# Kernel tuning notes

Measured on AMD Instinct MI355X. Metric: run time of the kernel, lower is better.

Reference implementation:

```python
import jax, jax.numpy as jnp
import numpy as np

N_NODES = 100000
N_EDGES = 1600000
IN_DIM = 256
OUT_DIM = 128


def setup_inputs() -> dict:
    key = jax.random.key(0)
    k1, k2, k3, k4, k5 = jax.random.split(key, 5)
    inputs = jax.random.normal(k1, (N_NODES, IN_DIM), dtype=jnp.float32)
    # xavier_uniform with relu gain, as in the torch init
    gain = float(np.sqrt(2.0))
    limit = gain * float(np.sqrt(6.0 / (IN_DIM + OUT_DIM)))
    W = jax.random.uniform(k2, (IN_DIM, OUT_DIM), dtype=jnp.float32,
                           minval=-limit, maxval=limit)
    edge_src = jax.random.randint(k3, (N_EDGES,), 0, N_NODES, dtype=jnp.int32)
    edge_dst = jax.random.randint(k4, (N_EDGES,), 0, N_NODES, dtype=jnp.int32)
    edge_val = jax.random.uniform(k5, (N_EDGES,), dtype=jnp.float32)
    return {"inputs": inputs, "W": W, "edge_src": edge_src,
            "edge_dst": edge_dst, "edge_val": edge_val}


def reference(inputs, W, edge_src, edge_dst, edge_val):
    # x = inputs @ W  (dense GEMM)
    h = inputs @ W                                  # [N, OUT_DIM]
    # adj @ h  as SpMM over COO edges: out[d] += val * h[s]
    msg = edge_val[:, None] * h[edge_src]           # [E, OUT_DIM]
    agg = jax.ops.segment_sum(msg, edge_dst, num_segments=N_NODES)
    # act = ReLU, fused with SpMM output
    return jax.nn.relu(agg)
```

## Files before the change

### kernel.cpp

```cpp
#include <hip/hip_runtime.h>
#include <hip/hip_bf16.h>

#define N_NODES 100000
#define N_EDGES 1600000
#define IN_DIM  256
#define OUT_DIM 128

#define GEMM_ROWS   64
#define GEMM_BLOCKS ((N_NODES + GEMM_ROWS - 1) / GEMM_ROWS)

#define NBUCK   196
#define BSHIFT  9
#define BCAP    10240
#define BSTRIDE 16
#define EPB     2048
#define BIN_BLOCKS ((N_EDGES + EPB - 1) / EPB)

typedef __attribute__((ext_vector_type(8))) short bf16x8;
typedef __attribute__((ext_vector_type(4))) float f32x4;

__device__ __forceinline__ ushort f2bf(float f) {
    union { float f; unsigned u; } v; v.f = f;
    unsigned r = v.u + 0x7FFF + ((v.u >> 16) & 1);
    return (ushort)(r >> 16);
}
__device__ __forceinline__ float bflo(unsigned u) {
    union { unsigned u; float f; } v; v.u = u << 16; return v.f;
}
__device__ __forceinline__ float bfhi(unsigned u) {
    union { unsigned u; float f; } v; v.u = u & 0xFFFF0000u; return v.f;
}

__global__ __launch_bounds__(256) void pack_w(const float* __restrict__ W,
                                              ushort* __restrict__ Wp) {
    const int t = blockIdx.x * 256 + threadIdx.x;
    if (t >= 4096) return;
    const int kk = t >> 9, n = (t >> 6) & 7, l = t & 63;
    const int kbase = kk * 32 + (l >> 4) * 8;
    const int col   = n * 16 + (l & 15);
    ushort* o = Wp + (size_t)t * 8;
#pragma unroll
    for (int j = 0; j < 8; ++j)
        o[j] = f2bf(W[(size_t)(kbase + j) * OUT_DIM + col]);
}

__global__ __launch_bounds__(256) void gemm_coarse(const float* __restrict__ X,
                                                   const bf16x8* __restrict__ Bp,
                                                   ushort* __restrict__ H,
                                                   const int* __restrict__ esrc,
                                                   const int* __restrict__ edst,
                                                   const float* __restrict__ eval,
                                                   int* __restrict__ bcur,
                                                   int2* __restrict__ binned) {
    __shared__ ushort xt[GEMM_ROWS * IN_DIM];

    if (blockIdx.x >= GEMM_BLOCKS) {
        int*   cnt   = (int*)xt;
        int*   lbase = (int*)xt + 256;
        int*   sbase = (int*)xt + 512;
        int*   cur   = (int*)xt + 768;
        int2*  lrec  = (int2*)((char*)xt + 4096);
        unsigned char* lbid = (unsigned char*)xt + 20480;

        const int blk = blockIdx.x - GEMM_BLOCKS;
        const int cb  = blk * EPB;
        const int lim = (N_EDGES - cb < EPB) ? (N_EDGES - cb) : EPB;
        const int tid = threadIdx.x;
        const int lane = tid & 63, wv = tid >> 6;

        if (tid < NBUCK) cnt[tid] = 0;
        __syncthreads();
        for (int i = tid; i < lim; i += 256)
            atomicAdd(&cnt[edst[cb + i] >> BSHIFT], 1);
        __syncthreads();

        {
            __shared__ int wsum[4];
            const int v = (tid < NBUCK) ? cnt[tid] : 0;
            int sv = v;
#pragma unroll
            for (int d = 1; d < 64; d <<= 1) {
                const int t = __shfl_up(sv, d, 64);
                if (lane >= d) sv += t;
            }
            if (lane == 63) wsum[wv] = sv;
            __syncthreads();
            int wx = 0;
#pragma unroll
            for (int w = 0; w < 4; ++w) if (w < wv) wx += wsum[w];
            if (tid < NBUCK) {
                const int ex = wx + sv - v;
                lbase[tid] = ex;
                cur[tid]   = ex;
                sbase[tid] = v ? atomicAdd(&bcur[tid * BSTRIDE], v) : 0;
            }
        }
        __syncthreads();

        for (int i = tid; i < lim; i += 256) {
            const int d = edst[cb + i];
            const int b = d >> BSHIFT;
            const int pos = atomicAdd(&cur[b], 1);
            int2 rec;
            rec.x = esrc[cb + i] | ((d & 511) << 20);
            rec.y = __float_as_int(eval[cb + i]);
            lrec[pos] = rec;
            lbid[pos] = (unsigned char)b;
        }
        __syncthreads();

        for (int i = tid; i < lim; i += 256) {
            const int b   = lbid[i];
            const int off = sbase[b] + (i - lbase[b]);
            if (off < BCAP)
                binned[(size_t)b * BCAP + off] = lrec[i];
        }
        return;
    }

    const int row0 = blockIdx.x * GEMM_ROWS;
    const int tid  = threadIdx.x;

    float4 v[16];
#pragma unroll
    for (int it = 0; it < 16; ++it) {
        const int tr = it * 4 + (tid >> 6);
        int grow = row0 + tr; if (grow >= N_NODES) grow = N_NODES - 1;
        v[it] = *reinterpret_cast<const float4*>(X + (size_t)grow * IN_DIM + (tid & 63) * 4);
    }
#pragma unroll
    for (int it = 0; it < 16; ++it) {
        const int tr = it * 4 + (tid >> 6);
        const int tc = (tid & 63) * 4;
        ushort4 b4;
        b4.x = f2bf(v[it].x); b4.y = f2bf(v[it].y);
        b4.z = f2bf(v[it].z); b4.w = f2bf(v[it].w);
        const int byte = (tr * 512 + tc * 2) ^ ((tr & 7) << 4);
        *reinterpret_cast<ushort4*>((char*)xt + byte) = b4;
    }
    __syncthreads();

    const int lane = tid & 63;
    const int wid  = tid >> 6;
    const int wr   = wid >> 1;
    const int wc   = wid & 1;
    const int rlo  = lane & 15;
    const int kseg = lane >> 4;
    const int rl0  = wr * 32 + rlo;
    const int rl1  = rl0 + 16;
    const int rxor = (rlo & 7) << 4;

    f32x4 acc[2][4] = {};

    for (int kk = 0; kk < 8; ++kk) {
        const int cb2 = (kk * 64 + kseg * 16) ^ rxor;
        const bf16x8 A0 = *reinterpret_cast<const bf16x8*>((const char*)xt + rl0 * 512 + cb2);
        const bf16x8 A1 = *reinterpret_cast<const bf16x8*>((const char*)xt + rl1 * 512 + cb2);
        const bf16x8* bbase = Bp + (size_t)(kk * 8 + wc * 4) * 64 + lane;
#pragma unroll
        for (int n = 0; n < 4; ++n) {
            const bf16x8 Bf = bbase[(size_t)n * 64];
            acc[0][n] = __builtin_amdgcn_mfma_f32_16x16x32_bf16(A0, Bf, acc[0][n], 0, 0, 0);
            acc[1][n] = __builtin_amdgcn_mfma_f32_16x16x32_bf16(A1, Bf, acc[1][n], 0, 0, 0);
        }
    }

#pragma unroll
    for (int i = 0; i < 2; ++i) {
#pragma unroll
        for (int r = 0; r < 4; ++r) {
            const int row = row0 + wr * 32 + i * 16 + kseg * 4 + r;
            if (row < N_NODES) {
#pragma unroll
                for (int n = 0; n < 4; ++n)
                    H[(size_t)row * OUT_DIM + (wc * 4 + n) * 16 + rlo] = f2bf(acc[i][n][r]);
            }
        }
    }
}

__global__ __launch_bounds__(256) void scan_buckets(const int* __restrict__ bcur,
                                                    int* __restrict__ gbase) {
    __shared__ int ws[4];
    const int tid = threadIdx.x, lane = tid & 63, wid = tid >> 6;
    const int v = (tid < NBUCK) ? bcur[tid * BSTRIDE] : 0;
    int sv = v;
#pragma unroll
    for (int d = 1; d < 64; d <<= 1) {
        const int t = __shfl_up(sv, d, 64);
        if (lane >= d) sv += t;
    }
    if (lane == 63) ws[wid] = sv;
    __syncthreads();
    int wx = 0;
#pragma unroll
    for (int w = 0; w < 4; ++w) if (w < wid) wx += ws[w];
    if (tid < NBUCK) gbase[tid] = wx + sv - v;
}

__global__ __launch_bounds__(1024) void bin_fine(const int* __restrict__ bcur,
                                                 const int* __restrict__ gbase,
                                                 const int2* __restrict__ binned,
                                                 int* __restrict__ offsets,
                                                 int2* __restrict__ recs) {
    __shared__ int nh[512];
    __shared__ int cur[512];
    __shared__ int ws[4];
    const int b   = blockIdx.x;
    const int tid = threadIdx.x, lane = tid & 63, wid = tid >> 6;
    const int node0 = b << BSHIFT;
    int nn = N_NODES - node0; if (nn > 512) nn = 512;
    int size = bcur[b * BSTRIDE]; if (size > BCAP) size = BCAP;
    const int2* in = binned + (size_t)b * BCAP;
    const int base_out = gbase[b];

    if (tid < 512) nh[tid] = 0;
    __syncthreads();
    for (int k = tid; k < size; k += 1024)
        atomicAdd(&nh[(in[k].x >> 20) & 511], 1);
    __syncthreads();

    int a0 = 0, ts = 0, sv = 0;
    if (tid < 256) {
        a0 = nh[2 * tid];
        const int a1 = nh[2 * tid + 1];
        ts = a0 + a1;
        sv = ts;
#pragma unroll
        for (int d = 1; d < 64; d <<= 1) {
            const int t = __shfl_up(sv, d, 64);
            if (lane >= d) sv += t;
        }
        if (lane == 63) ws[wid] = sv;
    }
    __syncthreads();
    if (tid < 256) {
        int wx = 0;
#pragma unroll
        for (int w = 0; w < 4; ++w) if (w < wid) wx += ws[w];
        const int ex = wx + sv - ts;
        cur[2 * tid]     = base_out + ex;
        cur[2 * tid + 1] = base_out + ex + a0;
        if (2 * tid < nn)     offsets[node0 + 2 * tid]     = base_out + ex;
        if (2 * tid + 1 < nn) offsets[node0 + 2 * tid + 1] = base_out + ex + a0;
    }
    if (b == 0 && tid == 0) offsets[N_NODES] = N_EDGES;
    __syncthreads();

    for (int k = tid; k < size; k += 1024) {
        const int2 r = in[k];
        const int pos = atomicAdd(&cur[(r.x >> 20) & 511], 1);
        int2 o; o.x = r.x & 0xFFFFF; o.y = r.y;
        recs[pos] = o;
    }
}

__global__ __launch_bounds__(256) void spmm_pull(const ushort* __restrict__ H,
                                                 const int* __restrict__ offsets,
                                                 const int2* __restrict__ recs,
                                                 float* __restrict__ out) {
    const int tid   = threadIdx.x;
    const int lane  = tid & 63;
    const int g     = lane >> 4;
    const int c     = lane & 15;
    const int gwave = blockIdx.x * 4 + (tid >> 6);
    const int node  = gwave * 4 + g;
    if (node >= N_NODES) return;

    const int beg = offsets[node];
    const int end = offsets[node + 1];

    float a0 = 0.f, a1 = 0.f, a2 = 0.f, a3 = 0.f;
    float a4 = 0.f, a5 = 0.f, a6 = 0.f, a7 = 0.f;

    int e = beg;
    for (; e + 3 < end; e += 4) {
        const int2 r0 = recs[e + 0];
        const int2 r1 = recs[e + 1];
        const int2 r2 = recs[e + 2];
        const int2 r3 = recs[e + 3];
        const uint4 h0 = *((const uint4*)(H + (size_t)r0.x * OUT_DIM) + c);
        const uint4 h1 = *((const uint4*)(H + (size_t)r1.x * OUT_DIM) + c);
        const uint4 h2 = *((const uint4*)(H + (size_t)r2.x * OUT_DIM) + c);
        const uint4 h3 = *((const uint4*)(H + (size_t)r3.x * OUT_DIM) + c);
        const float v0 = __int_as_float(r0.y), v1 = __int_as_float(r1.y);
        const float v2 = __int_as_float(r2.y), v3 = __int_as_float(r3.y);
        a0 = fmaf(v0, bflo(h0.x), a0);  a1 = fmaf(v0, bfhi(h0.x), a1);
        a2 = fmaf(v0, bflo(h0.y), a2);  a3 = fmaf(v0, bfhi(h0.y), a3);
        a4 = fmaf(v0, bflo(h0.z), a4);  a5 = fmaf(v0, bfhi(h0.z), a5);
        a6 = fmaf(v0, bflo(h0.w), a6);  a7 = fmaf(v0, bfhi(h0.w), a7);
        a0 = fmaf(v1, bflo(h1.x), a0);  a1 = fmaf(v1, bfhi(h1.x), a1);
        a2 = fmaf(v1, bflo(h1.y), a2);  a3 = fmaf(v1, bfhi(h1.y), a3);
        a4 = fmaf(v1, bflo(h1.z), a4);  a5 = fmaf(v1, bfhi(h1.z), a5);
        a6 = fmaf(v1, bflo(h1.w), a6);  a7 = fmaf(v1, bfhi(h1.w), a7);
        a0 = fmaf(v2, bflo(h2.x), a0);  a1 = fmaf(v2, bfhi(h2.x), a1);
        a2 = fmaf(v2, bflo(h2.y), a2);  a3 = fmaf(v2, bfhi(h2.y), a3);
        a4 = fmaf(v2, bflo(h2.z), a4);  a5 = fmaf(v2, bfhi(h2.z), a5);
        a6 = fmaf(v2, bflo(h2.w), a6);  a7 = fmaf(v2, bfhi(h2.w), a7);
        a0 = fmaf(v3, bflo(h3.x), a0);  a1 = fmaf(v3, bfhi(h3.x), a1);
        a2 = fmaf(v3, bflo(h3.y), a2);  a3 = fmaf(v3, bfhi(h3.y), a3);
        a4 = fmaf(v3, bflo(h3.z), a4);  a5 = fmaf(v3, bfhi(h3.z), a5);
        a6 = fmaf(v3, bflo(h3.w), a6);  a7 = fmaf(v3, bfhi(h3.w), a7);
    }
    for (; e < end; ++e) {
        const int2 r0 = recs[e];
        const float v0 = __int_as_float(r0.y);
        const uint4 h0 = *((const uint4*)(H + (size_t)r0.x * OUT_DIM) + c);
        a0 = fmaf(v0, bflo(h0.x), a0);  a1 = fmaf(v0, bfhi(h0.x), a1);
        a2 = fmaf(v0, bflo(h0.y), a2);  a3 = fmaf(v0, bfhi(h0.y), a3);
        a4 = fmaf(v0, bflo(h0.z), a4);  a5 = fmaf(v0, bfhi(h0.z), a5);
        a6 = fmaf(v0, bflo(h0.w), a6);  a7 = fmaf(v0, bfhi(h0.w), a7);
    }

    float* op = out + (size_t)node * OUT_DIM + c * 8;
    float4 o0, o1;
    o0.x = fmaxf(a0, 0.f); o0.y = fmaxf(a1, 0.f);
    o0.z = fmaxf(a2, 0.f); o0.w = fmaxf(a3, 0.f);
    o1.x = fmaxf(a4, 0.f); o1.y = fmaxf(a5, 0.f);
    o1.z = fmaxf(a6, 0.f); o1.w = fmaxf(a7, 0.f);
    *reinterpret_cast<float4*>(op)     = o0;
    *reinterpret_cast<float4*>(op + 4) = o1;
}

extern "C" void kernel_launch(void* const* d_in, const int* in_sizes, int n_in,
                              void* d_out, int out_size, void* d_ws, size_t ws_size,
                              hipStream_t stream) {
    const float* X    = (const float*)d_in[0];
    const float* W    = (const float*)d_in[1];
    const int*   esrc = (const int*)d_in[2];
    const int*   edst = (const int*)d_in[3];
    const float* eval = (const float*)d_in[4];
    float*       out  = (float*)d_out;

    char* ws = (char*)d_ws;
    ushort* Hb     = (ushort*)ws;  ws += (size_t)N_NODES * OUT_DIM * sizeof(ushort);
    ushort* Wp     = (ushort*)ws;  ws += (size_t)4096 * 8 * sizeof(ushort);
    int*    offsets= (int*)ws;     ws += (((size_t)(N_NODES + 1) * 4 + 127) & ~(size_t)127);
    int*    bcur   = (int*)ws;     ws += (size_t)NBUCK * BSTRIDE * 4;
    int*    gbase  = (int*)ws;     ws += ((NBUCK * 4 + 127) & ~127);
    int2*   binned = (int2*)ws;    ws += (size_t)NBUCK * BCAP * sizeof(int2);
    int2*   recs   = (int2*)ws;

    pack_w<<<16, 256, 0, stream>>>(W, Wp);
    hipMemsetAsync(bcur, 0, (size_t)NBUCK * BSTRIDE * 4, stream);
    gemm_coarse<<<GEMM_BLOCKS + BIN_BLOCKS, 256, 0, stream>>>(X, (const bf16x8*)Wp, Hb,
                                                              esrc, edst, eval,
                                                              bcur, binned);

    scan_buckets<<<1, 256, 0, stream>>>(bcur, gbase);
    bin_fine<<<NBUCK, 1024, 0, stream>>>(bcur, gbase, binned, offsets, recs);

    spmm_pull<<<(N_NODES + 15) / 16, 256, 0, stream>>>(Hb, offsets, recs, out);
}
```

Before: 134.4 us.

## Halve GEMM and binning tiles and raise occupancy of the fused kernel

The GEMM tile shrinks from 64 to 32 rows and now uses four waves that each cover 32 output columns, so each block needs less shared memory and fewer registers. Launch bounds now request 8 blocks per SM. The edge-binning blocks process 1024 edges each instead of 2048, with the LDS offsets adjusted to the smaller buffer. The X load loop now streams loads instead of preloading 16 float4s, and row bounds checks are dropped because 32 divides N_NODES exactly. In exchange there are more blocks, more total reads of the packed W, and more binning blocks that each add to the global atomic traffic.

```diff
diff --git a/kernel.cpp b/kernel.cpp
--- a/kernel.cpp
+++ b/kernel.cpp
@@ -6,14 +6,14 @@
 #define IN_DIM  256
 #define OUT_DIM 128
 
-#define GEMM_ROWS   64
-#define GEMM_BLOCKS ((N_NODES + GEMM_ROWS - 1) / GEMM_ROWS)
+#define GEMM_ROWS   32
+#define GEMM_BLOCKS (N_NODES / GEMM_ROWS)
 
 #define NBUCK   196
 #define BSHIFT  9
 #define BCAP    10240
 #define BSTRIDE 16
-#define EPB     2048
+#define EPB     1024
 #define BIN_BLOCKS ((N_EDGES + EPB - 1) / EPB)
 
 typedef __attribute__((ext_vector_type(8))) short bf16x8;
@@ -44,15 +44,15 @@
         o[j] = f2bf(W[(size_t)(kbase + j) * OUT_DIM + col]);
 }
 
-__global__ __launch_bounds__(256) void gemm_coarse(const float* __restrict__ X,
-                                                   const bf16x8* __restrict__ Bp,
-                                                   ushort* __restrict__ H,
-                                                   const int* __restrict__ esrc,
-                                                   const int* __restrict__ edst,
-                                                   const float* __restrict__ eval,
-                                                   int* __restrict__ bcur,
-                                                   int2* __restrict__ binned) {
-    __shared__ ushort xt[GEMM_ROWS * IN_DIM];
+__global__ __launch_bounds__(256, 8) void gemm_coarse(const float* __restrict__ X,
+                                                      const bf16x8* __restrict__ Bp,
+                                                      ushort* __restrict__ H,
+                                                      const int* __restrict__ esrc,
+                                                      const int* __restrict__ edst,
+                                                      const float* __restrict__ eval,
+                                                      int* __restrict__ bcur,
+                                                      int2* __restrict__ binned) {
+    __shared__ ushort xt[GEMM_ROWS * IN_DIM + 128];
 
     if (blockIdx.x >= GEMM_BLOCKS) {
         int*   cnt   = (int*)xt;
@@ -60,7 +60,7 @@
         int*   sbase = (int*)xt + 512;
         int*   cur   = (int*)xt + 768;
         int2*  lrec  = (int2*)((char*)xt + 4096);
-        unsigned char* lbid = (unsigned char*)xt + 20480;
+        unsigned char* lbid = (unsigned char*)xt + 12288;
 
         const int blk = blockIdx.x - GEMM_BLOCKS;
         const int cb  = blk * EPB;
@@ -121,20 +121,14 @@
     const int row0 = blockIdx.x * GEMM_ROWS;
     const int tid  = threadIdx.x;
 
-    float4 v[16];
-#pragma unroll
-    for (int it = 0; it < 16; ++it) {
-        const int tr = it * 4 + (tid >> 6);
-        int grow = row0 + tr; if (grow >= N_NODES) grow = N_NODES - 1;
-        v[it] = *reinterpret_cast<const float4*>(X + (size_t)grow * IN_DIM + (tid & 63) * 4);
-    }
-#pragma unroll
-    for (int it = 0; it < 16; ++it) {
+#pragma unroll 4
+    for (int it = 0; it < 8; ++it) {
         const int tr = it * 4 + (tid >> 6);
         const int tc = (tid & 63) * 4;
+        const float4 v = *reinterpret_cast<const float4*>(
+            X + (size_t)(row0 + tr) * IN_DIM + tc);
         ushort4 b4;
-        b4.x = f2bf(v[it].x); b4.y = f2bf(v[it].y);
-        b4.z = f2bf(v[it].z); b4.w = f2bf(v[it].w);
+        b4.x = f2bf(v.x); b4.y = f2bf(v.y); b4.z = f2bf(v.z); b4.w = f2bf(v.w);
         const int byte = (tr * 512 + tc * 2) ^ ((tr & 7) << 4);
         *reinterpret_cast<ushort4*>((char*)xt + byte) = b4;
     }
@@ -142,23 +136,21 @@
 
     const int lane = tid & 63;
     const int wid  = tid >> 6;
-    const int wr   = wid >> 1;
-    const int wc   = wid & 1;
     const int rlo  = lane & 15;
     const int kseg = lane >> 4;
-    const int rl0  = wr * 32 + rlo;
-    const int rl1  = rl0 + 16;
+    const int rl0  = rlo;
+    const int rl1  = rlo + 16;
     const int rxor = (rlo & 7) << 4;
 
-    f32x4 acc[2][4] = {};
+    f32x4 acc[2][2] = {};
 
     for (int kk = 0; kk < 8; ++kk) {
         const int cb2 = (kk * 64 + kseg * 16) ^ rxor;
         const bf16x8 A0 = *reinterpret_cast<const bf16x8*>((const char*)xt + rl0 * 512 + cb2);
         const bf16x8 A1 = *reinterpret_cast<const bf16x8*>((const char*)xt + rl1 * 512 + cb2);
-        const bf16x8* bbase = Bp + (size_t)(kk * 8 + wc * 4) * 64 + lane;
-#pragma unroll
-        for (int n = 0; n < 4; ++n) {
+        const bf16x8* bbase = Bp + (size_t)(kk * 8 + wid * 2) * 64 + lane;
+#pragma unroll
+        for (int n = 0; n < 2; ++n) {
             const bf16x8 Bf = bbase[(size_t)n * 64];
             acc[0][n] = __builtin_amdgcn_mfma_f32_16x16x32_bf16(A0, Bf, acc[0][n], 0, 0, 0);
             acc[1][n] = __builtin_amdgcn_mfma_f32_16x16x32_bf16(A1, Bf, acc[1][n], 0, 0, 0);
@@ -166,17 +158,13 @@
     }
 
 #pragma unroll
-    for (int i = 0; i < 2; ++i) {
-#pragma unroll
-        for (int r = 0; r < 4; ++r) {
-            const int row = row0 + wr * 32 + i * 16 + kseg * 4 + r;
-            if (row < N_NODES) {
-#pragma unroll
-                for (int n = 0; n < 4; ++n)
-                    H[(size_t)row * OUT_DIM + (wc * 4 + n) * 16 + rlo] = f2bf(acc[i][n][r]);
-            }
-        }
-    }
+    for (int i = 0; i < 2; ++i)
+#pragma unroll
+        for (int r = 0; r < 4; ++r)
+#pragma unroll
+            for (int n = 0; n < 2; ++n)
+                H[(size_t)(row0 + i * 16 + kseg * 4 + r) * OUT_DIM
+                  + wid * 32 + n * 16 + rlo] = f2bf(acc[i][n][r]);
 }
 
 __global__ __launch_bounds__(256) void scan_buckets(const int* __restrict__ bcur,
```

Measured after the change: 142.6 us. +6.1%, slower.
